# Optimization experiments

Measured on AMD Instinct MI355X. Metric: run time of the kernel, lower is better.

## Reference

```python
import jax, jax.numpy as jnp
import numpy as np

VOCAB = 50000
NUM_TAGS = 12
EMBED_DIM = 300
HIDDEN_DIM = 300
B, S = 64, 256
START_IDX = NUM_TAGS - 2
STOP_IDX = NUM_TAGS - 1
NEG = -10000.0


def setup_inputs() -> dict:
    key = jax.random.key(0)
    ks = jax.random.split(key, 12)
    # tokens in [1, VOCAB) so mask = (sentences != 0) is all ones (full-length, sorted)
    sentences = jax.random.randint(ks[0], (B, S), 1, VOCAB)
    tags = jax.random.randint(ks[1], (B, S), 0, NUM_TAGS)
    embed_table = jax.random.normal(ks[2], (VOCAB, EMBED_DIM), jnp.float32)
    k = 1.0 / np.sqrt(HIDDEN_DIM)
    u = lambda kk, shp: jax.random.uniform(kk, shp, jnp.float32, -k, k)
    # PyTorch LSTM gate order: i, f, g, o. b = b_ih + b_hh fused.
    W_ih_f = u(ks[3], (4 * HIDDEN_DIM, EMBED_DIM))
    W_hh_f = u(ks[4], (4 * HIDDEN_DIM, HIDDEN_DIM))
    b_f = u(ks[5], (4 * HIDDEN_DIM,))
    W_ih_b = u(ks[6], (4 * HIDDEN_DIM, EMBED_DIM))
    W_hh_b = u(ks[7], (4 * HIDDEN_DIM, HIDDEN_DIM))
    b_b = u(ks[8], (4 * HIDDEN_DIM,))
    kl = 1.0 / np.sqrt(2 * HIDDEN_DIM)
    W_lin = jax.random.uniform(ks[9], (NUM_TAGS, 2 * HIDDEN_DIM), jnp.float32, -kl, kl)
    b_lin = jax.random.uniform(ks[10], (NUM_TAGS,), jnp.float32, -kl, kl)
    transitions = jax.random.uniform(ks[11], (NUM_TAGS, NUM_TAGS), jnp.float32)
    transitions = transitions.at[START_IDX, :].set(NEG)
    transitions = transitions.at[:, STOP_IDX].set(NEG)
    return dict(sentences=sentences, tags=tags, embed_table=embed_table,
                W_ih_f=W_ih_f, W_hh_f=W_hh_f, b_f=b_f,
                W_ih_b=W_ih_b, W_hh_b=W_hh_b, b_b=b_b,
                W_lin=W_lin, b_lin=b_lin, transitions=transitions)


def _lstm_scan(x_seq, W_ih, W_hh, b):
    # x_seq: (S, B, E) -> (S, B, H)
    H = W_hh.shape[1]
    Bb = x_seq.shape[1]

    def step(carry, x_t):
        h, c = carry
        g = x_t @ W_ih.T + h @ W_hh.T + b
        i, f, gg, o = jnp.split(g, 4, axis=-1)
        c = jax.nn.sigmoid(f) * c + jax.nn.sigmoid(i) * jnp.tanh(gg)
        h = jax.nn.sigmoid(o) * jnp.tanh(c)
        return (h, c), h

    init = (jnp.zeros((Bb, H), x_seq.dtype), jnp.zeros((Bb, H), x_seq.dtype))
    _, hs = jax.lax.scan(step, init, x_seq)
    return hs


def reference(sentences, tags, embed_table, W_ih_f, W_hh_f, b_f,
              W_ih_b, W_hh_b, b_b, W_lin, b_lin, transitions):
    # Embedding, time-major layout (S, B, E)
    x = embed_table[sentences].transpose(1, 0, 2)
    h_f = _lstm_scan(x, W_ih_f, W_hh_f, b_f)
    h_b = jnp.flip(_lstm_scan(jnp.flip(x, 0), W_ih_b, W_hh_b, b_b), 0)
    lstm_out = jnp.concatenate([h_f, h_b], axis=-1)          # (S, B, 2H)
    emit = lstm_out @ W_lin.T + b_lin                         # (S, B, K)
    emit_bsk = emit.transpose(1, 0, 2)                        # (B, S, K)

    # Gold path score (mask is all ones for full-length sequences)
    tok_score = jnp.take_along_axis(emit_bsk, tags[..., None], axis=2).squeeze(2)
    trans_score = transitions[tags[:, :-1], tags[:, 1:]]
    total_score = tok_score.sum(axis=1) + trans_score.sum(axis=1)

    # CRF partition function: forward algorithm over time
    def crf_step(d, e_t):
        # d: (B, K) prev log-alpha; e_t: (B, K) emissions at step t
        # log_sum[b, j, k] = d[b, j] + trans[j, k] + e_t[b, k]
        d_new = jax.nn.logsumexp(d[:, :, None] + transitions[None] + e_t[:, None, :], axis=1)
        return d_new, None

    d0 = emit[0]                                              # (B, K)
    d_final, _ = jax.lax.scan(crf_step, d0, emit[1:])
    log_z = jax.nn.logsumexp(d_final, axis=1)                 # (B,)

    loss = log_z - total_score                                # -log-likelihood per example
    return loss
```

## Files before the change

### kernel.cpp

```cpp
#include <hip/hip_runtime.h>
#include <hip/hip_bf16.h>

static constexpr int BATCH = 64;
static constexpr int SEQ   = 256;
static constexpr int ED    = 300;
static constexpr int HD    = 300;
static constexpr int HPAD  = 320;
static constexpr int GPAD  = 1280;
static constexpr int NTAG  = 12;
static constexpr int NWG_DIR = 10;
static constexpr int NH      = 32;

static constexpr size_t O_GIN  = 0;
static constexpr size_t SZ_GIN = (size_t)2*SEQ*BATCH*GPAD*2;
static constexpr size_t O_H    = O_GIN + SZ_GIN;
static constexpr size_t SZ_H   = (size_t)2*SEQ*NWG_DIR*BATCH*NH*2;
static constexpr size_t O_WHH  = O_H + SZ_H;
static constexpr size_t SZ_WHH = (size_t)2*GPAD*HPAD*2;
static constexpr size_t O_WIH  = O_WHH + SZ_WHH;
static constexpr size_t SZ_WIH = (size_t)2*GPAD*HPAD*2;
static constexpr size_t O_BIAS = O_WIH + SZ_WIH;
static constexpr size_t SZ_BIAS= (size_t)2*GPAD*4;
static constexpr size_t O_EMIT = O_BIAS + SZ_BIAS;
static constexpr size_t SZ_EMIT= (size_t)SEQ*BATCH*NTAG*4;
static constexpr size_t O_CTR  = O_EMIT + SZ_EMIT;

typedef __bf16 bf16x8 __attribute__((ext_vector_type(8)));
typedef float  f32x4  __attribute__((ext_vector_type(4)));
typedef unsigned short u16x8 __attribute__((ext_vector_type(8)));
typedef unsigned short u16;

__device__ __forceinline__ float bu(u16 u){ union{unsigned i; float f;} x; x.i = ((unsigned)u)<<16; return x.f; }
__device__ __forceinline__ u16 fb(float f){ union{float f; unsigned i;} x; x.f = f; unsigned r = x.i + 0x7FFFu + ((x.i>>16)&1u); return (u16)(r>>16); }
__device__ __forceinline__ float sigf(float x){ return 1.0f/(1.0f + __expf(-x)); }
__device__ __forceinline__ float tanh_(float x){ return 2.0f*sigf(2.0f*x) - 1.0f; }
__device__ __forceinline__ f32x4 mfma16(bf16x8 a, bf16x8 b, f32x4 c){
  return __builtin_amdgcn_mfma_f32_16x16x32_bf16(a, b, c, 0, 0, 0);
}
__device__ __forceinline__ int swz4(int r){ return ((r + (r>>2)) & 3); }

__global__ __launch_bounds__(256) void k0_pack(
    const float* whf, const float* whb, const float* wif, const float* wib,
    const float* bfv, const float* bbv,
    u16* wpkhh, u16* wpkih, float* biasPk, int* flags)
{
  int idx = blockIdx.x*256 + threadIdx.x;
  int mat = idx / (2*GPAD*HPAD);
  int rem = idx % (2*GPAD*HPAD);
  int dd  = rem / (GPAD*HPAD);
  int rr  = rem % (GPAD*HPAD);
  int R   = rr / HPAD, kk = rr % HPAD;
  int jj  = R >> 2, gate = R & 3;
  float v = 0.f;
  if (jj < HD && kk < HD){
    const float* src = mat ? (dd ? wib : wif) : (dd ? whb : whf);
    v = src[(size_t)(gate*HD + jj)*ED + kk];
  }
  (mat ? wpkih : wpkhh)[rem] = fb(v);
  if (idx < 2*GPAD){
    int d2 = idx / GPAD, R2 = idx % GPAD;
    int j2 = R2 >> 2, g2 = R2 & 3;
    biasPk[idx] = (j2 < HD) ? (d2 ? bbv : bfv)[g2*HD + j2] : 0.f;
  }
  if (idx < 2*NWG_DIR*16) flags[idx] = 0;
}

__global__ __launch_bounds__(256) void k1_gin(
    const int* sent, const float* embed, const u16* wpkih,
    const float* biasPk, u16* gin)
{
  int blk = blockIdx.x;
  int mb = blk / 40, nb = blk % 40;
  int tid = threadIdx.x, lane = tid & 63, w = tid >> 6;

  __shared__ int srow[64];
  __shared__ u16 sA[64*32];
  __shared__ u16 sB[64*32];

  if (tid < 64) srow[tid] = sent[(size_t)tid*SEQ + mb];
  __syncthreads();

  f32x4 acc[4] = {f32x4{0,0,0,0},f32x4{0,0,0,0},f32x4{0,0,0,0},f32x4{0,0,0,0}};
  int r = tid >> 2, cc = tid & 3;
  int col = lane & 15, hi = lane >> 4;

  for (int k0 = 0; k0 < 10; k0++){
    {
      int kbase = k0*32 + cc*8;
      const float* erow = embed + (size_t)srow[r]*ED;
      float v[8];
      if (kbase + 8 <= ED){
        float4 p0 = *(const float4*)(erow + kbase);
        float4 p1 = *(const float4*)(erow + kbase + 4);
        v[0]=p0.x; v[1]=p0.y; v[2]=p0.z; v[3]=p0.w;
        v[4]=p1.x; v[5]=p1.y; v[6]=p1.z; v[7]=p1.w;
      } else {
        #pragma unroll
        for (int e = 0; e < 8; e++) v[e] = (kbase + e < ED) ? erow[kbase + e] : 0.f;
      }
      u16x8 pk;
      #pragma unroll
      for (int e = 0; e < 8; e++) pk[e] = fb(v[e]);
      *(u16x8*)&sA[r*32 + ((cc ^ swz4(r))*8)] = pk;
      int n = nb*64 + r;
      u16x8 bv = *(const u16x8*)(wpkih + (size_t)n*HPAD + k0*32 + cc*8);
      *(u16x8*)&sB[r*32 + ((cc ^ swz4(r))*8)] = bv;
    }
    __syncthreads();
    {
      int ar = w*16 + col;
      bf16x8 a = *(const bf16x8*)&sA[ar*32 + ((hi ^ swz4(ar))*8)];
      #pragma unroll
      for (int nt = 0; nt < 4; nt++){
        int br = nt*16 + col;
        bf16x8 b = *(const bf16x8*)&sB[br*32 + ((hi ^ swz4(br))*8)];
        acc[nt] = mfma16(a, b, acc[nt]);
      }
    }
    __syncthreads();
  }
  #pragma unroll
  for (int nt = 0; nt < 4; nt++){
    int n_g = nb*64 + nt*16 + col;
    int d = n_g / GPAD, R = n_g % GPAD;
    float bias = biasPk[n_g];
    #pragma unroll
    for (int reg = 0; reg < 4; reg++){
      int b = w*16 + hi*4 + reg;
      float val = acc[nt][reg] + bias;
      gin[(((size_t)d*SEQ + mb)*BATCH + b)*GPAD + R] = fb(val);
    }
  }
}

__global__ __launch_bounds__(256,1) void k2_lstm(
    const u16* wpkhh, const u16* gin, u16* hbuf, int* flags)
{
  const int tid = threadIdx.x, lane = tid & 63, wid = tid >> 6;
  const int d = blockIdx.x / NWG_DIR, sl = blockIdx.x % NWG_DIR;
  const int mi = wid >> 1, ni = wid & 1;
  const int col = lane & 15, hi = lane >> 4;
  const int gb = tid >> 2, jq = tid & 3;

  __shared__ __align__(16) char smem[40960];
  u16*   sH = (u16*)smem;
  float* sG = (float*)smem;

  bf16x8 Bf[10][4];
  #pragma unroll
  for (int k = 0; k < 10; k++)
    #pragma unroll
    for (int nt = 0; nt < 4; nt++){
      size_t off = ((size_t)d*GPAD + sl*128 + ni*64 + nt*16 + col)*HPAD + k*32 + hi*8;
      Bf[k][nt] = *(const bf16x8*)(wpkhh + off);
    }

  float cst[8];
  #pragma unroll
  for (int q = 0; q < 8; q++) cst[q] = 0.f;

  int* myflag = flags + (d*NWG_DIR + sl)*16;

  for (int rstep = 0; rstep < SEQ; rstep++){
    int t_store = d ? (SEQ-1-rstep) : rstep;

    u16x8 gv[4];
    {
      const u16* gq = gin + (((size_t)d*SEQ + t_store)*BATCH + gb)*GPAD + sl*128 + jq*32;
      #pragma unroll
      for (int m = 0; m < 4; m++) gv[m] = *(const u16x8*)(gq + m*8);
    }

    if (rstep > 0){
      if (tid < NWG_DIR){
        const int* fp = flags + (d*NWG_DIR + tid)*16;
        while (__hip_atomic_load(fp, __ATOMIC_RELAXED, __HIP_MEMORY_SCOPE_AGENT) < rstep)
          __builtin_amdgcn_s_sleep(1);
      }
      __syncthreads();
      __builtin_amdgcn_fence(__ATOMIC_ACQUIRE, "agent");

      int t_prev = d ? (t_store+1) : (rstep-1);
      const u16* hsrc = hbuf + (size_t)(d*SEQ + t_prev)*NWG_DIR*BATCH*NH;
      #pragma unroll
      for (int q = 0; q < 10; q++){
        int f = q*256 + tid;
        int b = (f >> 2) & 63;
        int cch = ((f >> 8) << 2) + (f & 3);
        u16x8 v = *(const u16x8*)(hsrc + (size_t)f*8);
        *(u16x8*)&sH[b*320 + ((cch ^ (b&7))*8)] = v;
      }
      __syncthreads();
      f32x4 acc[2][4];
      #pragma unroll
      for (int mt = 0; mt < 2; mt++)
        #pragma unroll
        for (int nt = 0; nt < 4; nt++) acc[mt][nt] = f32x4{0,0,0,0};
      #pragma unroll
      for (int k = 0; k < 10; k++){
        int c = k*4 + hi;
        int r0 = mi*32 + col, r1 = r0 + 16;
        bf16x8 a0 = *(const bf16x8*)&sH[r0*320 + ((c ^ (r0&7))*8)];
        bf16x8 a1 = *(const bf16x8*)&sH[r1*320 + ((c ^ (r1&7))*8)];
        #pragma unroll
        for (int nt = 0; nt < 4; nt++){
          acc[0][nt] = mfma16(a0, Bf[k][nt], acc[0][nt]);
          acc[1][nt] = mfma16(a1, Bf[k][nt], acc[1][nt]);
        }
      }
      __syncthreads();
      #pragma unroll
      for (int mt = 0; mt < 2; mt++)
        #pragma unroll
        for (int nt = 0; nt < 4; nt++){
          int nl = ni*64 + nt*16 + col;
          int bb = mi*32 + mt*16 + hi*4;
          #pragma unroll
          for (int g = 0; g < 4; g++) sG[(bb+g)*133 + nl] = acc[mt][nt][g];
        }
      __syncthreads();
    }

    u16x8 hout;
    #pragma unroll
    for (int ji = 0; ji < 8; ji++){
      float i_ = bu(gv[(ji>>1)][ (ji&1)*4 + 0 ]);
      float f_ = bu(gv[(ji>>1)][ (ji&1)*4 + 1 ]);
      float g_ = bu(gv[(ji>>1)][ (ji&1)*4 + 2 ]);
      float o_ = bu(gv[(ji>>1)][ (ji&1)*4 + 3 ]);
      if (rstep > 0){
        f32x4 r = *(const f32x4*)&sG[gb*133 + (jq*8 + ji)*4];
        i_ += r[0]; f_ += r[1]; g_ += r[2]; o_ += r[3];
      }
      float cn = sigf(f_)*cst[ji] + sigf(i_)*tanh_(g_);
      cst[ji] = cn;
      hout[ji] = (u16)fb(sigf(o_)*tanh_(cn));
    }
    {
      u16* hdst = hbuf + ((size_t)(d*SEQ + t_store)*NWG_DIR + sl)*BATCH*NH + gb*NH + jq*8;
      union { u16x8 v; unsigned w[4]; } hu; hu.v = hout;
      unsigned* hd = (unsigned*)hdst;
      #pragma unroll
      for (int m = 0; m < 4; m++)
        __hip_atomic_store(hd + m, hu.w[m], __ATOMIC_RELAXED, __HIP_MEMORY_SCOPE_AGENT);
    }
    __syncthreads();
    if (tid == 0)
      __hip_atomic_store(myflag, rstep + 1, __ATOMIC_RELEASE, __HIP_MEMORY_SCOPE_AGENT);
  }
}

__global__ __launch_bounds__(256) void k3_emit(
    const u16* hbuf, const float* wlin, const float* blin, float* emit)
{
  int blk = blockIdx.x;
  int t = blk >> 1, b0 = (blk & 1)*32;
  int tid = threadIdx.x;

  __shared__ u16 sh[32*600];
  __shared__ u16 swl[NTAG*600];
  __shared__ float sbl[NTAG];

  for (int p = tid; p < NTAG*600; p += 256) swl[p] = fb(wlin[p]);
  if (tid < NTAG) sbl[tid] = blin[tid];
  for (int p = tid; p < 32*600; p += 256){
    int b = p / 600, c = p % 600;
    int dd = (c < HD) ? 0 : 1;
    int c2 = (c < HD) ? c : (c - HD);
    int sl = c2 >> 5, j = c2 & 31;
    u16 v = hbuf[((size_t)(dd*SEQ + t)*NWG_DIR + sl)*BATCH*NH + (b0 + b)*NH + j];
    sh[p] = v;
  }
  __syncthreads();

  for (int p = tid; p < 32*NTAG; p += 256){
    int b = p & 31, k = p >> 5;
    const u16x8* ha = (const u16x8*)&sh[b*600];
    const u16x8* wa = (const u16x8*)&swl[k*600];
    float s = 0.f;
    #pragma unroll 5
    for (int c = 0; c < 75; c++){
      u16x8 hv = ha[c], wv = wa[c];
      #pragma unroll
      for (int e = 0; e < 8; e++) s += bu(hv[e])*bu(wv[e]);
    }
    emit[((size_t)t*BATCH + b0 + b)*NTAG + k] = s + sbl[k];
  }
}

__global__ __launch_bounds__(256) void k4_crf(
    const float* emit, const int* tags, const float* trans, float* out)
{
  int b0 = blockIdx.x*16;
  int tid = threadIdx.x;
  __shared__ float sT[NTAG*NTAG];
  __shared__ float sd[2][16][NTAG];

  if (tid < NTAG*NTAG) sT[tid] = trans[tid];
  int b = tid / NTAG, k = tid % NTAG;
  bool act = tid < 16*NTAG;
  if (act) sd[0][b][k] = emit[((size_t)0*BATCH + b0 + b)*NTAG + k];
  __syncthreads();

  int cur = 0;
  for (int t = 1; t < SEQ; t++){
    if (act){
      float m = -1e30f;
      #pragma unroll
      for (int j = 0; j < NTAG; j++) m = fmaxf(m, sd[cur][b][j] + sT[j*NTAG + k]);
      float ssum = 0.f;
      #pragma unroll
      for (int j = 0; j < NTAG; j++) ssum += __expf(sd[cur][b][j] + sT[j*NTAG + k] - m);
      sd[cur^1][b][k] = m + __logf(ssum) + emit[((size_t)t*BATCH + b0 + b)*NTAG + k];
    }
    __syncthreads();
    cur ^= 1;
  }

  if (tid < 16){
    int bb = b0 + tid;
    const int* tg = tags + (size_t)bb*SEQ;
    float sc = 0.f; int prev = tg[0];
    sc += emit[((size_t)0*BATCH + bb)*NTAG + prev];
    for (int t = 1; t < SEQ; t++){
      int c2 = tg[t];
      sc += emit[((size_t)t*BATCH + bb)*NTAG + c2] + sT[prev*NTAG + c2];
      prev = c2;
    }
    float m = -1e30f;
    for (int k2 = 0; k2 < NTAG; k2++) m = fmaxf(m, sd[cur][tid][k2]);
    float ssum = 0.f;
    for (int k2 = 0; k2 < NTAG; k2++) ssum += __expf(sd[cur][tid][k2] - m);
    out[bb] = m + __logf(ssum) - sc;
  }
}

extern "C" void kernel_launch(void* const* d_in, const int* in_sizes, int n_in,
                              void* d_out, int out_size, void* d_ws, size_t ws_size,
                              hipStream_t stream)
{
  const int*   sent  = (const int*)  d_in[0];
  const int*   tags  = (const int*)  d_in[1];
  const float* embed = (const float*)d_in[2];
  const float* wif   = (const float*)d_in[3];
  const float* whf   = (const float*)d_in[4];
  const float* bfv   = (const float*)d_in[5];
  const float* wib   = (const float*)d_in[6];
  const float* whb   = (const float*)d_in[7];
  const float* bbv   = (const float*)d_in[8];
  const float* wlin  = (const float*)d_in[9];
  const float* blin  = (const float*)d_in[10];
  const float* trans = (const float*)d_in[11];

  char* ws = (char*)d_ws;
  u16*   gin    = (u16*)  (ws + O_GIN);
  u16*   hbuf   = (u16*)  (ws + O_H);
  u16*   wpkhh  = (u16*)  (ws + O_WHH);
  u16*   wpkih  = (u16*)  (ws + O_WIH);
  float* biasPk = (float*)(ws + O_BIAS);
  float* emit   = (float*)(ws + O_EMIT);
  int*   flags  = (int*)  (ws + O_CTR);

  k0_pack<<<6400, 256, 0, stream>>>(whf, whb, wif, wib, bfv, bbv,
                                    wpkhh, wpkih, biasPk, flags);
  k1_gin<<<256*40, 256, 0, stream>>>(sent, embed, wpkih, biasPk, gin);
  k2_lstm<<<2*NWG_DIR, 256, 0, stream>>>(wpkhh, gin, hbuf, flags);
  k3_emit<<<SEQ*2, 256, 0, stream>>>(hbuf, wlin, blin, emit);
  k4_crf<<<4, 256, 0, stream>>>(emit, tags, trans, (float*)d_out);
}
```

Before: 2.290 ms.

## Stage recurrent weights in LDS, prefetch next-step gate inputs, use plain h stores

The W_hh slice each workgroup needs is now copied once into a swizzled 80KB LDS buffer and read from there every step, instead of being held as 160 VGPRs of bf16 fragments. This frees register pressure at the cost of extra LDS reads per MFMA. The precomputed input-gate values for the next timestep are loaded one step ahead, so the global load latency overlaps with the current step's spin-wait and matmul. The per-dword relaxed atomic stores of h are replaced by a single vector store, which relies on the release fence on the flag for visibility.

```diff
diff --git a/kernel.cpp b/kernel.cpp
--- a/kernel.cpp
+++ b/kernel.cpp
@@ -142,18 +142,22 @@
   const int col = lane & 15, hi = lane >> 4;
   const int gb = tid >> 2, jq = tid & 3;
 
-  __shared__ __align__(16) char smem[40960];
-  u16*   sH = (u16*)smem;
-  float* sG = (float*)smem;
-
-  bf16x8 Bf[10][4];
-  #pragma unroll
-  for (int k = 0; k < 10; k++)
-    #pragma unroll
-    for (int nt = 0; nt < 4; nt++){
-      size_t off = ((size_t)d*GPAD + sl*128 + ni*64 + nt*16 + col)*HPAD + k*32 + hi*8;
-      Bf[k][nt] = *(const bf16x8*)(wpkhh + off);
-    }
+  __shared__ __align__(16) char smem[122880];
+  u16*   sW = (u16*)smem;
+  u16*   sH = (u16*)(smem + 81920);
+  float* sG = (float*)(smem + 81920);
+
+  {
+    const u16* wsrc = wpkhh + ((size_t)d*GPAD + sl*128)*HPAD;
+    #pragma unroll
+    for (int q = 0; q < 20; q++){
+      int f = q*256 + tid;
+      int r = f / 40, c = f % 40;
+      u16x8 v = *(const u16x8*)(wsrc + (size_t)r*HPAD + c*8);
+      *(u16x8*)&sW[(r*40 + (c ^ (r & 7)))*8] = v;
+    }
+  }
+  __syncthreads();
 
   float cst[8];
   #pragma unroll
@@ -161,14 +165,22 @@
 
   int* myflag = flags + (d*NWG_DIR + sl)*16;
 
+  u16x8 gvA[4], gvB[4];
+  {
+    int t0 = d ? (SEQ-1) : 0;
+    const u16* gq = gin + (((size_t)d*SEQ + t0)*BATCH + gb)*GPAD + sl*128 + jq*32;
+    #pragma unroll
+    for (int m = 0; m < 4; m++) gvA[m] = *(const u16x8*)(gq + m*8);
+  }
+
   for (int rstep = 0; rstep < SEQ; rstep++){
     int t_store = d ? (SEQ-1-rstep) : rstep;
 
-    u16x8 gv[4];
-    {
-      const u16* gq = gin + (((size_t)d*SEQ + t_store)*BATCH + gb)*GPAD + sl*128 + jq*32;
-      #pragma unroll
-      for (int m = 0; m < 4; m++) gv[m] = *(const u16x8*)(gq + m*8);
+    if (rstep + 1 < SEQ){
+      int t1 = d ? (SEQ-2-rstep) : (rstep+1);
+      const u16* gq = gin + (((size_t)d*SEQ + t1)*BATCH + gb)*GPAD + sl*128 + jq*32;
+      #pragma unroll
+      for (int m = 0; m < 4; m++) gvB[m] = *(const u16x8*)(gq + m*8);
     }
 
     if (rstep > 0){
@@ -204,8 +216,10 @@
         bf16x8 a1 = *(const bf16x8*)&sH[r1*320 + ((c ^ (r1&7))*8)];
         #pragma unroll
         for (int nt = 0; nt < 4; nt++){
-          acc[0][nt] = mfma16(a0, Bf[k][nt], acc[0][nt]);
-          acc[1][nt] = mfma16(a1, Bf[k][nt], acc[1][nt]);
+          int rb = ni*64 + nt*16 + col;
+          bf16x8 b = *(const bf16x8*)&sW[(rb*40 + (c ^ (rb & 7)))*8];
+          acc[0][nt] = mfma16(a0, b, acc[0][nt]);
+          acc[1][nt] = mfma16(a1, b, acc[1][nt]);
         }
       }
       __syncthreads();
@@ -224,10 +238,10 @@
     u16x8 hout;
     #pragma unroll
     for (int ji = 0; ji < 8; ji++){
-      float i_ = bu(gv[(ji>>1)][ (ji&1)*4 + 0 ]);
-      float f_ = bu(gv[(ji>>1)][ (ji&1)*4 + 1 ]);
-      float g_ = bu(gv[(ji>>1)][ (ji&1)*4 + 2 ]);
-      float o_ = bu(gv[(ji>>1)][ (ji&1)*4 + 3 ]);
+      float i_ = bu(gvA[(ji>>1)][ (ji&1)*4 + 0 ]);
+      float f_ = bu(gvA[(ji>>1)][ (ji&1)*4 + 1 ]);
+      float g_ = bu(gvA[(ji>>1)][ (ji&1)*4 + 2 ]);
+      float o_ = bu(gvA[(ji>>1)][ (ji&1)*4 + 3 ]);
       if (rstep > 0){
         f32x4 r = *(const f32x4*)&sG[gb*133 + (jq*8 + ji)*4];
         i_ += r[0]; f_ += r[1]; g_ += r[2]; o_ += r[3];
@@ -238,15 +252,14 @@
     }
     {
       u16* hdst = hbuf + ((size_t)(d*SEQ + t_store)*NWG_DIR + sl)*BATCH*NH + gb*NH + jq*8;
-      union { u16x8 v; unsigned w[4]; } hu; hu.v = hout;
-      unsigned* hd = (unsigned*)hdst;
-      #pragma unroll
-      for (int m = 0; m < 4; m++)
-        __hip_atomic_store(hd + m, hu.w[m], __ATOMIC_RELAXED, __HIP_MEMORY_SCOPE_AGENT);
+      *(u16x8*)hdst = hout;
     }
     __syncthreads();
     if (tid == 0)
       __hip_atomic_store(myflag, rstep + 1, __ATOMIC_RELEASE, __HIP_MEMORY_SCOPE_AGENT);
+
+    #pragma unroll
+    for (int m = 0; m < 4; m++) gvA[m] = gvB[m];
   }
 }
 
```

After: 1.858 ms. 1.23x faster.
